# Kernel tuning notes

Hardware: AMD Instinct MI355X
Metric: run time of the kernel (lower is better)

The kernel has to match this reference:

```python
import jax, jax.numpy as jnp
import numpy as np

B, L, D, H = 2, 4096, 512, 8
HD = D // H  # head_dim = 64


def setup_inputs() -> dict:
    key = jax.random.key(0)
    ks = jax.random.split(key, 5)
    s = 0.02
    return {
        "x": jax.random.normal(ks[0], (B, L, D), dtype=jnp.float32),
        "w_qkv": jax.random.normal(ks[1], (D, 3 * D), dtype=jnp.float32) * s,
        "b_qkv": jax.random.normal(ks[2], (3 * D,), dtype=jnp.float32) * s,
        "w_o": jax.random.normal(ks[3], (D, D), dtype=jnp.float32) * s,
        "b_o": jax.random.normal(ks[4], (D,), dtype=jnp.float32) * s,
    }


def reference(x, w_qkv, b_qkv, w_o, b_o):
    b, l, _ = x.shape
    # QKV projection, then split heads: [B, L, 3D] -> [B, H, L, 3*HD]
    qkv = x @ w_qkv + b_qkv
    qkv = qkv.reshape(b, l, H, 3 * HD).transpose(0, 2, 1, 3)
    q, k, v = jnp.split(qkv, 3, axis=-1)  # each [B, H, L, HD]
    scale = 1.0 / jnp.sqrt(jnp.asarray(HD, dtype=q.dtype))
    # full score matrix [B, H, L, L], softmax in float32 (matches .float() cast)
    scores = jnp.einsum('bhld,bhsd->bhls', q, k) * scale
    attn = jax.nn.softmax(scores.astype(jnp.float32), axis=-1).astype(q.dtype)
    values = jnp.einsum('bhls,bhsd->bhld', attn, v)  # [B, H, L, HD]
    values = values.transpose(0, 2, 1, 3).reshape(b, l, D)
    return values @ w_o + b_o
```

## Files before the change

### kernel.cpp

```cpp
#include <hip/hip_runtime.h>


#define B_  2
#define L_  4096
#define D_  512
#define H_  8
#define HD_ 64
#define BH_ (B_*H_)
#define M_  (B_*L_)
#define QKVN (3*D_)
#define HEADSZ (BH_*L_*HD_)

typedef unsigned short ushort;
typedef unsigned int uint;
typedef __bf16 bf16x8 __attribute__((ext_vector_type(8)));
typedef float  f32x4  __attribute__((ext_vector_type(4)));
typedef float  f32x16 __attribute__((ext_vector_type(16)));

typedef const __attribute__((address_space(1))) void g_void;
typedef __attribute__((address_space(3))) void l_void;

#define C2_ 0.18033688011112042f

__device__ __forceinline__ ushort f2bf(float f) {
    __bf16 h = (__bf16)f;
    return __builtin_bit_cast(ushort, h);
}

__device__ __forceinline__ uint pack2(float lo, float hi) {
    return (uint)f2bf(lo) | ((uint)f2bf(hi) << 16);
}

__global__ __launch_bounds__(256)
void prep_k(const float* __restrict__ x, ushort* __restrict__ xb,
            const float* __restrict__ wq, ushort* __restrict__ wtq,
            const float* __restrict__ wo, ushort* __restrict__ wto)
{
    int bid = blockIdx.x, tid = threadIdx.x;
    if (bid < 4096) {
        int idx = bid * 256 + tid;
        float4 v = ((const float4*)x)[idx];
        ushort4 o; o.x = f2bf(v.x); o.y = f2bf(v.y); o.z = f2bf(v.z); o.w = f2bf(v.w);
        ((ushort4*)xb)[idx] = o;
    } else if (bid < 7168) {
        int idx = (bid - 4096) * 256 + tid;
        int c = idx / D_, r = idx % D_;
        wtq[idx] = f2bf(wq[r * QKVN + c]);
    } else {
        int idx = (bid - 7168) * 256 + tid;
        int c = idx / D_, r = idx % D_;
        wto[idx] = f2bf(wo[r * D_ + c]);
    }
}

#define TP 66
__global__ __launch_bounds__(256)
void transpose_v(const ushort* __restrict__ V, ushort* __restrict__ VT) {
    __shared__ ushort T[64 * TP];
    const int tid = threadIdx.x;
    const int bh = blockIdx.y;
    const int l0 = blockIdx.x * 64;
    const int base = bh * (L_ * HD_);
    #pragma unroll
    for (int i = 0; i < 2; i++) {
        int c = i * 256 + tid;
        int l = c >> 3, dc = (c & 7) * 8;
        uint4 v = *(const uint4*)&V[base + (l0 + l) * HD_ + dc];
        uint* p = (uint*)&T[l * TP + dc];
        p[0] = v.x; p[1] = v.y; p[2] = v.z; p[3] = v.w;
    }
    __syncthreads();
    #pragma unroll
    for (int p = 0; p < 2; p++) {
        int c = p * 256 + tid;
        int d = c >> 3, lb = c & 7;
        ushort tmp[8];
        #pragma unroll
        for (int j = 0; j < 8; j++) tmp[j] = T[(lb * 8 + j) * TP + d];
        *(uint4*)&VT[base + d * L_ + l0 + lb * 8] = *(uint4*)tmp;
    }
}

__global__ __launch_bounds__(256)
void gemm_bt(const ushort* __restrict__ A, const ushort* __restrict__ Bt,
             const float* __restrict__ bias, void* __restrict__ out,
             int M, int N, int K, int mode)
{
    __shared__ ushort As[128 * 32];
    __shared__ ushort Bs[128 * 32];

    const int tid  = threadIdx.x;
    const int lane = tid & 63;
    const int wid  = tid >> 6;
    const int wm   = wid >> 1, wn = wid & 1;
    const int lr   = lane & 15;
    const int quad = lane >> 4;
    const int tm = blockIdx.x, tn = blockIdx.y;

    f32x4 acc[4][4] = {};
    const int arow = tm * 128;
    const int brow = tn * 128;

    for (int k0 = 0; k0 < K; k0 += 32) {
        #pragma unroll
        for (int i = 0; i < 2; i++) {
            int c   = i * 256 + tid;
            int row = c >> 2;
            int kk  = (c & 3) * 8;
            __builtin_amdgcn_global_load_lds(
                (g_void*)&A[(size_t)(arow + row) * K + k0 + kk],
                (l_void*)&As[c * 8], 16, 0, 0);
            __builtin_amdgcn_global_load_lds(
                (g_void*)&Bt[(size_t)(brow + row) * K + k0 + kk],
                (l_void*)&Bs[c * 8], 16, 0, 0);
        }
        __syncthreads();

        bf16x8 af[4], bfr[4];
        #pragma unroll
        for (int t = 0; t < 4; t++) {
            af [t] = *(const bf16x8*)&As[(wm * 64 + t * 16 + lr) * 32 + quad * 8];
            bfr[t] = *(const bf16x8*)&Bs[(wn * 64 + t * 16 + lr) * 32 + quad * 8];
        }
        #pragma unroll
        for (int mt = 0; mt < 4; mt++)
            #pragma unroll
            for (int nt = 0; nt < 4; nt++)
                acc[mt][nt] = __builtin_amdgcn_mfma_f32_16x16x32_bf16(
                    af[mt], bfr[nt], acc[mt][nt], 0, 0, 0);
        __syncthreads();
    }

    #pragma unroll
    for (int nt = 0; nt < 4; nt++) {
        int col = tn * 128 + wn * 64 + nt * 16 + lr;
        float bv = bias[col];
        #pragma unroll
        for (int mt = 0; mt < 4; mt++) {
            #pragma unroll
            for (int r = 0; r < 4; r++) {
                int row = tm * 128 + wm * 64 + mt * 16 + quad * 4 + r;
                float v = acc[mt][nt][r] + bv;
                if (mode == 0) {
                    ((float*)out)[(size_t)row * N + col] = v;
                } else {
                    int d = col & 63;
                    int g = col >> 6;
                    int which = g % 3;
                    int h = g / 3;
                    int b = row >> 12;
                    int l = row & (L_ - 1);
                    if (which == 0) v *= C2_;
                    ((ushort*)out)[which * HEADSZ + (((b * H_ + h) * L_ + l) * HD_) + d]
                        = f2bf(v);
                }
            }
        }
    }
}

__global__ __launch_bounds__(256)
void attn_k(const ushort* __restrict__ Q, const ushort* __restrict__ K,
            const ushort* __restrict__ VT, ushort* __restrict__ O)
{
    __shared__ __align__(16) ushort Ks[2][64 * 64];
    __shared__ __align__(16) ushort Vt[2][64 * 64];
    __shared__ float Linv[4][32];

    const int tid  = threadIdx.x;
    const int lane = tid & 63;
    const int wid  = tid >> 6;
    const int l31  = lane & 31;
    const int hi   = lane >> 5;

    const int wg  = blockIdx.x;
    const int xcd = wg & 7, sl = wg >> 3;
    const int bh  = (xcd << 1) | (sl >> 5);
    const int q0  = (sl & 31) * 128;
    const size_t base = (size_t)bh * (L_ * HD_);

    const int sr0 = tid >> 3,        sr1 = (tid + 256) >> 3;
    const int sc0 = ((tid & 7) ^ (sr0 & 7)) * 8;
    const int sc1 = ((tid & 7) ^ (sr1 & 7)) * 8;
    const ushort* Kg0 = K  + base + sr0 * HD_ + sc0;
    const ushort* Kg1 = K  + base + sr1 * HD_ + sc1;
    const ushort* Vg0 = VT + base + (size_t)sr0 * L_ + sc0;
    const ushort* Vg1 = VT + base + (size_t)sr1 * L_ + sc1;

    bf16x8 qf[4];
    {
        const ushort* qp = Q + base + (size_t)(q0 + wid * 32 + l31) * HD_ + hi * 8;
        #pragma unroll
        for (int ks = 0; ks < 4; ks++) qf[ks] = *(const bf16x8*)(qp + ks * 16);
    }

    const int swz = (l31 & 7) << 4;
    int cbe[4];
    #pragma unroll
    for (int ks = 0; ks < 4; ks++) cbe[ks] = ((ks * 32 + hi * 16) ^ swz) >> 1;
    const int kr0 = l31 * 64, kr1 = (32 + l31) * 64;

    __builtin_amdgcn_global_load_lds((g_void*)Kg0, (l_void*)&Ks[0][tid * 8], 16, 0, 0);
    __builtin_amdgcn_global_load_lds((g_void*)Kg1, (l_void*)&Ks[0][tid * 8 + 2048], 16, 0, 0);
    __builtin_amdgcn_global_load_lds((g_void*)Vg0, (l_void*)&Vt[0][tid * 8], 16, 0, 0);
    __builtin_amdgcn_global_load_lds((g_void*)Vg1, (l_void*)&Vt[0][tid * 8 + 2048], 16, 0, 0);

    f32x16 o0 = {}, o1 = {};
    float l4[4] = {0.f, 0.f, 0.f, 0.f};

    for (int t = 0; t < L_ / 64; t++) {
        const int cur = t & 1;
        __syncthreads();

        if (t + 1 < L_ / 64) {
            const size_t ko = (size_t)(t + 1) * 64 * HD_;
            const int    vo = (t + 1) * 64;
            __builtin_amdgcn_global_load_lds(
                (g_void*)(Kg0 + ko), (l_void*)&Ks[cur ^ 1][tid * 8], 16, 0, 0);
            __builtin_amdgcn_global_load_lds(
                (g_void*)(Kg1 + ko), (l_void*)&Ks[cur ^ 1][tid * 8 + 2048], 16, 0, 0);
            __builtin_amdgcn_global_load_lds(
                (g_void*)(Vg0 + vo), (l_void*)&Vt[cur ^ 1][tid * 8], 16, 0, 0);
            __builtin_amdgcn_global_load_lds(
                (g_void*)(Vg1 + vo), (l_void*)&Vt[cur ^ 1][tid * 8 + 2048], 16, 0, 0);
        }

        f32x16 sA = {}, sB = {};
        __builtin_amdgcn_s_setprio(1);
        #pragma unroll
        for (int ks = 0; ks < 4; ks++) {
            bf16x8 k0 = *(const bf16x8*)&Ks[cur][kr0 + cbe[ks]];
            bf16x8 k1 = *(const bf16x8*)&Ks[cur][kr1 + cbe[ks]];
            sA = __builtin_amdgcn_mfma_f32_32x32x16_bf16(k0, qf[ks], sA, 0, 0, 0);
            sB = __builtin_amdgcn_mfma_f32_32x32x16_bf16(k1, qf[ks], sB, 0, 0, 0);
        }
        __builtin_amdgcn_s_setprio(0);

        #pragma unroll
        for (int i = 0; i < 16; i++) { sA[i] = exp2f(sA[i]); sB[i] = exp2f(sB[i]); }
        #pragma unroll
        for (int i = 0; i < 16; i++) l4[i & 3] += sA[i] + sB[i];

        __builtin_amdgcn_s_setprio(1);
        #pragma unroll
        for (int ks = 0; ks < 4; ks++) {
            const f32x16& P = (ks >> 1) ? sB : sA;
            const int r0 = 8 * (ks & 1);
            uint a0 = pack2(P[r0 + 0], P[r0 + 1]);
            uint a1 = pack2(P[r0 + 2], P[r0 + 3]);
            uint b0 = pack2(P[r0 + 4], P[r0 + 5]);
            uint b1 = pack2(P[r0 + 6], P[r0 + 7]);
            asm("v_permlane32_swap_b32 %0, %1" : "+v"(a0), "+v"(b0));
            asm("v_permlane32_swap_b32 %0, %1" : "+v"(a1), "+v"(b1));
            uint4 w; w.x = a0; w.y = a1; w.z = b0; w.w = b1;
            bf16x8 pa = __builtin_bit_cast(bf16x8, w);
            bf16x8 v0 = *(const bf16x8*)&Vt[cur][kr0 + cbe[ks]];
            bf16x8 v1 = *(const bf16x8*)&Vt[cur][kr1 + cbe[ks]];
            o0 = __builtin_amdgcn_mfma_f32_32x32x16_bf16(pa, v0, o0, 0, 0, 0);
            o1 = __builtin_amdgcn_mfma_f32_32x32x16_bf16(pa, v1, o1, 0, 0, 0);
        }
        __builtin_amdgcn_s_setprio(0);
    }

    float lp = (l4[0] + l4[1]) + (l4[2] + l4[3]);
    lp += __shfl_xor(lp, 32, 64);
    if (hi == 0) Linv[wid][l31] = 1.0f / lp;

    const int b = bh >> 3, h = bh & 7;
    #pragma unroll
    for (int r = 0; r < 16; r++) {
        const int qrl = (r & 3) + 8 * (r >> 2) + 4 * hi;
        const float inv = Linv[wid][qrl];
        const size_t row = (size_t)(b * L_ + q0 + wid * 32 + qrl) * D_ + h * HD_ + l31;
        O[row]      = f2bf(o0[r] * inv);
        O[row + 32] = f2bf(o1[r] * inv);
    }
}

extern "C" void kernel_launch(void* const* d_in, const int* in_sizes, int n_in,
                              void* d_out, int out_size, void* d_ws, size_t ws_size,
                              hipStream_t stream)
{
    const float* x     = (const float*)d_in[0];
    const float* w_qkv = (const float*)d_in[1];
    const float* b_qkv = (const float*)d_in[2];
    const float* w_o   = (const float*)d_in[3];
    const float* b_o   = (const float*)d_in[4];

    char* ws = (char*)d_ws;
    size_t o = 0;
    ushort* xb   = (ushort*)(ws + o); o += (size_t)M_ * D_ * 2;
    ushort* qkv  = (ushort*)(ws + o); o += (size_t)3 * HEADSZ * 2;
    ushort* attn = (ushort*)(ws + o); o += (size_t)M_ * D_ * 2;
    ushort* wtq  = (ushort*)(ws + o); o += (size_t)QKVN * D_ * 2;
    ushort* wto  = (ushort*)(ws + o);
    ushort* vt   = xb;

    hipLaunchKernelGGL(prep_k, dim3(8192), dim3(256), 0, stream,
                       x, xb, w_qkv, wtq, w_o, wto);
    hipLaunchKernelGGL(gemm_bt, dim3(M_ / 128, QKVN / 128), dim3(256), 0, stream,
                       xb, wtq, b_qkv, (void*)qkv, M_, QKVN, D_, 1);
    hipLaunchKernelGGL(transpose_v, dim3(L_ / 64, BH_), dim3(256), 0, stream,
                       qkv + 2 * HEADSZ, vt);
    hipLaunchKernelGGL(attn_k, dim3(512), dim3(256), 0, stream,
                       qkv, qkv + HEADSZ, vt, attn);
    hipLaunchKernelGGL(gemm_bt, dim3(M_ / 128, D_ / 128), dim3(256), 0, stream,
                       attn, wto, b_o, d_out, M_, D_, D_, 0);
}
```

Baseline: 244.0 us.

## Software-pipeline attention loop so QK of next tile overlaps softmax/PV of previous

Restructures the attention inner loop into a two-stage software pipeline. The QK^T MFMAs for tile t run alongside the exp2/PV work for tile t-1, using separate even/odd score registers. V is given a 4-deep LDS ring so the previous tile's V stays resident while new tiles stream in. The goal is to hide exp latency and MFMA dependency stalls, at the cost of more VGPRs for the extra score accumulators, more LDS, and dropping the s_setprio hints.

```diff
diff --git a/kernel.cpp b/kernel.cpp
--- a/kernel.cpp
+++ b/kernel.cpp
@@ -163,8 +163,8 @@
 void attn_k(const ushort* __restrict__ Q, const ushort* __restrict__ K,
             const ushort* __restrict__ VT, ushort* __restrict__ O)
 {
-    __shared__ __align__(16) ushort Ks[2][64 * 64];
-    __shared__ __align__(16) ushort Vt[2][64 * 64];
+    __shared__ __align__(16) ushort Ksm[2][64 * 64];
+    __shared__ __align__(16) ushort Vsm[4][64 * 64];
     __shared__ float Linv[4][32];
 
     const int tid  = threadIdx.x;
@@ -200,51 +200,42 @@
     for (int ks = 0; ks < 4; ks++) cbe[ks] = ((ks * 32 + hi * 16) ^ swz) >> 1;
     const int kr0 = l31 * 64, kr1 = (32 + l31) * 64;
 
-    __builtin_amdgcn_global_load_lds((g_void*)Kg0, (l_void*)&Ks[0][tid * 8], 16, 0, 0);
-    __builtin_amdgcn_global_load_lds((g_void*)Kg1, (l_void*)&Ks[0][tid * 8 + 2048], 16, 0, 0);
-    __builtin_amdgcn_global_load_lds((g_void*)Vg0, (l_void*)&Vt[0][tid * 8], 16, 0, 0);
-    __builtin_amdgcn_global_load_lds((g_void*)Vg1, (l_void*)&Vt[0][tid * 8 + 2048], 16, 0, 0);
-
     f32x16 o0 = {}, o1 = {};
+    f32x16 sEA, sEB, sOA, sOB;
     float l4[4] = {0.f, 0.f, 0.f, 0.f};
 
-    for (int t = 0; t < L_ / 64; t++) {
-        const int cur = t & 1;
-        __syncthreads();
-
-        if (t + 1 < L_ / 64) {
-            const size_t ko = (size_t)(t + 1) * 64 * HD_;
-            const int    vo = (t + 1) * 64;
-            __builtin_amdgcn_global_load_lds(
-                (g_void*)(Kg0 + ko), (l_void*)&Ks[cur ^ 1][tid * 8], 16, 0, 0);
-            __builtin_amdgcn_global_load_lds(
-                (g_void*)(Kg1 + ko), (l_void*)&Ks[cur ^ 1][tid * 8 + 2048], 16, 0, 0);
-            __builtin_amdgcn_global_load_lds(
-                (g_void*)(Vg0 + vo), (l_void*)&Vt[cur ^ 1][tid * 8], 16, 0, 0);
-            __builtin_amdgcn_global_load_lds(
-                (g_void*)(Vg1 + vo), (l_void*)&Vt[cur ^ 1][tid * 8 + 2048], 16, 0, 0);
-        }
-
-        f32x16 sA = {}, sB = {};
-        __builtin_amdgcn_s_setprio(1);
+    auto STAGE = [&](int tt) {
+        const size_t ko = (size_t)tt * 64 * HD_;
+        const int    vo = tt * 64;
+        ushort* kb = &Ksm[tt & 1][0];
+        ushort* vb = &Vsm[tt & 3][0];
+        __builtin_amdgcn_global_load_lds((g_void*)(Kg0 + ko), (l_void*)(kb + tid * 8),        16, 0, 0);
+        __builtin_amdgcn_global_load_lds((g_void*)(Kg1 + ko), (l_void*)(kb + tid * 8 + 2048), 16, 0, 0);
+        __builtin_amdgcn_global_load_lds((g_void*)(Vg0 + vo), (l_void*)(vb + tid * 8),        16, 0, 0);
+        __builtin_amdgcn_global_load_lds((g_void*)(Vg1 + vo), (l_void*)(vb + tid * 8 + 2048), 16, 0, 0);
+    };
+
+    auto QK = [&](int tt, f32x16& SA, f32x16& SB) {
+        const ushort* kb = &Ksm[tt & 1][0];
+        SA = f32x16{}; SB = f32x16{};
         #pragma unroll
         for (int ks = 0; ks < 4; ks++) {
-            bf16x8 k0 = *(const bf16x8*)&Ks[cur][kr0 + cbe[ks]];
-            bf16x8 k1 = *(const bf16x8*)&Ks[cur][kr1 + cbe[ks]];
-            sA = __builtin_amdgcn_mfma_f32_32x32x16_bf16(k0, qf[ks], sA, 0, 0, 0);
-            sB = __builtin_amdgcn_mfma_f32_32x32x16_bf16(k1, qf[ks], sB, 0, 0, 0);
-        }
-        __builtin_amdgcn_s_setprio(0);
-
-        #pragma unroll
-        for (int i = 0; i < 16; i++) { sA[i] = exp2f(sA[i]); sB[i] = exp2f(sB[i]); }
-        #pragma unroll
-        for (int i = 0; i < 16; i++) l4[i & 3] += sA[i] + sB[i];
-
-        __builtin_amdgcn_s_setprio(1);
+            bf16x8 k0 = *(const bf16x8*)&kb[kr0 + cbe[ks]];
+            bf16x8 k1 = *(const bf16x8*)&kb[kr1 + cbe[ks]];
+            SA = __builtin_amdgcn_mfma_f32_32x32x16_bf16(k0, qf[ks], SA, 0, 0, 0);
+            SB = __builtin_amdgcn_mfma_f32_32x32x16_bf16(k1, qf[ks], SB, 0, 0, 0);
+        }
+    };
+
+    auto SMPV = [&](int tp, f32x16& SA, f32x16& SB) {
+        const ushort* vb = &Vsm[tp & 3][0];
+        #pragma unroll
+        for (int i = 0; i < 16; i++) { SA[i] = exp2f(SA[i]); SB[i] = exp2f(SB[i]); }
+        #pragma unroll
+        for (int i = 0; i < 16; i++) l4[i & 3] += SA[i] + SB[i];
         #pragma unroll
         for (int ks = 0; ks < 4; ks++) {
-            const f32x16& P = (ks >> 1) ? sB : sA;
+            const f32x16& P = (ks >> 1) ? SB : SA;
             const int r0 = 8 * (ks & 1);
             uint a0 = pack2(P[r0 + 0], P[r0 + 1]);
             uint a1 = pack2(P[r0 + 2], P[r0 + 3]);
@@ -254,13 +245,26 @@
             asm("v_permlane32_swap_b32 %0, %1" : "+v"(a1), "+v"(b1));
             uint4 w; w.x = a0; w.y = a1; w.z = b0; w.w = b1;
             bf16x8 pa = __builtin_bit_cast(bf16x8, w);
-            bf16x8 v0 = *(const bf16x8*)&Vt[cur][kr0 + cbe[ks]];
-            bf16x8 v1 = *(const bf16x8*)&Vt[cur][kr1 + cbe[ks]];
+            bf16x8 v0 = *(const bf16x8*)&vb[kr0 + cbe[ks]];
+            bf16x8 v1 = *(const bf16x8*)&vb[kr1 + cbe[ks]];
             o0 = __builtin_amdgcn_mfma_f32_32x32x16_bf16(pa, v0, o0, 0, 0, 0);
             o1 = __builtin_amdgcn_mfma_f32_32x32x16_bf16(pa, v1, o1, 0, 0, 0);
         }
-        __builtin_amdgcn_s_setprio(0);
-    }
+    };
+
+    STAGE(0);
+
+    for (int t = 0; t < L_ / 64; t += 2) {
+        __syncthreads();
+        STAGE(t + 1);
+        QK(t, sEA, sEB);
+        if (t > 0) SMPV(t - 1, sOA, sOB);
+        __syncthreads();
+        if (t + 2 < L_ / 64) STAGE(t + 2);
+        QK(t + 1, sOA, sOB);
+        SMPV(t, sEA, sEB);
+    }
+    SMPV(L_ / 64 - 1, sOA, sOB);
 
     float lp = (l4[0] + l4[1]) + (l4[2] + l4[3]);
     lp += __shfl_xor(lp, 32, 64);
```

After: 236.0 us. 1.03x faster.
